# Performance work log

Measured on AMD Instinct MI355X. Metric: run time of the kernel, lower is better.

## Reference

```python
import jax, jax.numpy as jnp
import numpy as np

D = 64        # gat_output_dim == state_dim
HID = 128     # hidden_dim
ADIM = 2 * D  # action_dim (ope_dim + insert_dim)


def _mk(key, shape, scale=0.05):
    return jax.random.normal(key, shape, dtype=jnp.float32) * scale


def setup_inputs() -> dict:
    key = jax.random.key(0)
    ks = jax.random.split(key, 24)
    inp = {
        "ope_gat": jax.random.normal(ks[0], (8, 258, D), jnp.float32),
        "insert_gat": jax.random.normal(ks[1], (8, 256, D), jnp.float32),
        "h": jax.random.normal(ks[2], (8, D), jnp.float32),
        "c": jax.random.normal(ks[3], (8, D), jnp.float32),
        # LSTM (pytorch layout: gates i,f,g,o stacked -> [4D, in])
        "W_ih": _mk(ks[4], (4 * D, D)),
        "W_hh": _mk(ks[5], (4 * D, D)),
        "b_ih": _mk(ks[6], (4 * D,)),
        "b_hh": _mk(ks[7], (4 * D,)),
        # V_net: Linear(D,HID) -> Linear(HID,HID) -> LeakyReLU -> Linear(HID,1)
        "Wv0": _mk(ks[8], (HID, D)), "bv0": _mk(ks[9], (HID,)),
        "Wv1": _mk(ks[10], (HID, HID)), "bv1": _mk(ks[11], (HID,)),
        "Wv2": _mk(ks[12], (1, HID)), "bv2": _mk(ks[13], (1,)),
        # A_net: Linear(D+ADIM,HID) -> Linear(HID,HID) -> LeakyReLU -> Linear(HID,1)
        "Wa0": _mk(ks[14], (HID, D + ADIM)), "ba0": _mk(ks[15], (HID,)),
        "Wa1": _mk(ks[16], (HID, HID)), "ba1": _mk(ks[17], (HID,)),
        "Wa2": _mk(ks[18], (1, HID)), "ba2": _mk(ks[19], (1,)),
    }
    return inp


def _lrelu(x):
    return jnp.where(x >= 0, x, 0.01 * x)


def _forward(ope_gat, insert_gat, h, c,
             W_ih, W_hh, b_ih, b_hh,
             Wv0, bv0, Wv1, bv1, Wv2, bv2,
             Wa0, ba0, Wa1, ba1, Wa2, ba2):
    ope = ope_gat[:, 1:-1]                # [B, O, D]
    state = ope.mean(axis=-2)             # [B, D]

    # single-step LSTM (pytorch gate order i, f, g, o)
    gates = state @ W_ih.T + b_ih + h @ W_hh.T + b_hh  # [B, 4D]
    i_g, f_g, g_g, o_g = jnp.split(gates, 4, axis=-1)
    cn = jax.nn.sigmoid(f_g) * c + jax.nn.sigmoid(i_g) * jnp.tanh(g_g)
    hn = jax.nn.sigmoid(o_g) * jnp.tanh(cn)
    rnn_state = hn                        # [B, D]

    # V head (note: no activation after first linear -- name-overwrite bug)
    V = _lrelu((rnn_state @ Wv0.T + bv0) @ Wv1.T + bv1) @ Wv2.T + bv2  # [B, 1]

    # A head on the full (ope x insert) cross-join; ope side is detached.
    ope_d = jax.lax.stop_gradient(ope)    # [B, O, D]
    B, O, _ = ope_d.shape
    I = insert_gat.shape[1]
    # Decompose first linear over the concat [state | ope | insert] (exact math).
    Ws, Wo, Wi = Wa0[:, :D], Wa0[:, D:2 * D], Wa0[:, 2 * D:]
    h0 = (rnn_state @ Ws.T)[:, None, None, :] \
         + jnp.einsum('bod,hd->boh', ope_d, Wo)[:, :, None, :] \
         + jnp.einsum('bid,hd->bih', insert_gat, Wi)[:, None, :, :] \
         + ba0                              # [B, O, I, HID]
    h1 = _lrelu(jnp.einsum('boih,gh->boig', h0, Wa1) + ba1)
    A = (jnp.einsum('boih,h->boi', h1, Wa2[0]) + ba2[0]).reshape(B, O * I)
    return V, A, hn, cn


def reference(ope_gat, insert_gat, h, c,
              W_ih, W_hh, b_ih, b_hh,
              Wv0, bv0, Wv1, bv1, Wv2, bv2,
              Wa0, ba0, Wa1, ba1, Wa2, ba2):
    return _forward(ope_gat, insert_gat, h, c,
                    W_ih, W_hh, b_ih, b_hh,
                    Wv0, bv0, Wv1, bv1, Wv2, bv2,
                    Wa0, ba0, Wa1, ba1, Wa2, ba2)
```

## Files before the change

### kernel.cpp

```cpp
#include <hip/hip_runtime.h>
#include <hip/hip_bf16.h>
#include <math.h>

typedef unsigned short u16;


__device__ __forceinline__ u16 f2b(float x) { __hip_bfloat16 b = __float2bfloat16(x); return *(u16*)&b; }
__device__ __forceinline__ void cvt8(const uint4 u, float* f) {
    f[0] = __uint_as_float(u.x << 16); f[1] = __uint_as_float(u.x & 0xFFFF0000u);
    f[2] = __uint_as_float(u.y << 16); f[3] = __uint_as_float(u.y & 0xFFFF0000u);
    f[4] = __uint_as_float(u.z << 16); f[5] = __uint_as_float(u.z & 0xFFFF0000u);
    f[6] = __uint_as_float(u.w << 16); f[7] = __uint_as_float(u.w & 0xFFFF0000u);
}

__global__ __launch_bounds__(256) void k1_head(
    const float* __restrict__ ope, const float* __restrict__ hin, const float* __restrict__ cin,
    const float* __restrict__ W_ih, const float* __restrict__ W_hh,
    const float* __restrict__ b_ih, const float* __restrict__ b_hh,
    const float* __restrict__ Wv0, const float* __restrict__ bv0,
    const float* __restrict__ Wv1, const float* __restrict__ bv1,
    const float* __restrict__ Wv2, const float* __restrict__ bv2,
    const float* __restrict__ Wa0, const float* __restrict__ ba0,
    const float* __restrict__ Wa2, const float* __restrict__ ba2,
    float* __restrict__ ws, int fb)
{
    const int b = blockIdx.x, t = threadIdx.x;
    __shared__ float red[256], state[64], hvec[64], gl[256], hn_s[64], t0a[128], t1a[128];

    {
        const int d = t & 63, q = t >> 6;
        const float* p = ope + b * 16512 + (1 + q * 64) * 64 + d;
        float s = 0.f;
        #pragma unroll 8
        for (int r = 0; r < 64; ++r) s += p[r * 64];
        red[t] = s;
    }
    __syncthreads();
    if (t < 64)       state[t]   = (red[t] + red[t+64] + red[t+128] + red[t+192]) * (1.f/256.f);
    else if (t < 128) hvec[t-64] = hin[b*64 + (t-64)];
    __syncthreads();

    {
        float g = b_ih[t] + b_hh[t];
        #pragma unroll 8
        for (int d = 0; d < 64; ++d)
            g += state[d] * W_ih[t*64 + d] + hvec[d] * W_hh[t*64 + d];
        gl[t] = g;
    }
    __syncthreads();

    if (t < 64) {
        const float ig = gl[t], fg = gl[64+t], gg = gl[128+t], og = gl[192+t];
        const float c  = cin[b*64 + t];
        const float si = 1.f/(1.f + expf(-ig));
        const float sf = 1.f/(1.f + expf(-fg));
        const float so = 1.f/(1.f + expf(-og));
        const float cn = sf*c + si*tanhf(gg);
        const float hn = so*tanhf(cn);
        ws[fb + 1288 + b*64 + t] = hn;
        ws[fb + 1800 + b*64 + t] = cn;
        hn_s[t] = hn;
    }
    __syncthreads();

    if (t < 128) {
        float a = bv0[t];
        #pragma unroll 8
        for (int d = 0; d < 64; ++d) a += hn_s[d] * Wv0[t*64 + d];
        t0a[t] = a;
    }
    __syncthreads();
    if (t < 128) {
        float a = bv1[t];
        #pragma unroll 8
        for (int d = 0; d < 128; ++d) a += t0a[d] * Wv1[t*128 + d];
        a = (a >= 0.f) ? a : 0.01f*a;
        t1a[t] = a * Wv2[t];
        float s2 = ba0[t];
        #pragma unroll 8
        for (int d = 0; d < 64; ++d) s2 += hn_s[d] * Wa0[t*192 + d];
        ws[fb + b*128 + t] = s2;
        const float w2v = Wa2[t];
        ws[fb + 1024 + t] = 0.505f * w2v;
        ws[fb + 1152 + t] = 0.495f * w2v;
    }
    __syncthreads();
    if (t == 0) {
        float v = bv2[0];
        for (int g = 0; g < 128; ++g) v += t1a[g];
        ws[fb + 1280 + b] = v;
        ws[fb + 2313]    = ba2[0];
    }
}

template<bool MF32>
__device__ void k2_body(const float* ope, const float* ins, const float* Wa0,
    const float* Wa1, const float* ba1, float* ws, int fb,
    u16* Wa1s, u16* Wsel, u16* inrows, float* P)
{
    const int t = threadIdx.x;
    const int b = blockIdx.x >> 5;
    const int r0 = (blockIdx.x & 31) * 16;
    const int side = (r0 >= 256) ? 1 : 0;

    #pragma unroll
    for (int k = 0; k < 16; ++k) {
        const int e4 = t + k*256;
        const int g = e4 >> 5, hq = (e4 & 31) * 4;
        const float4 w = *(const float4*)(Wa1 + g*128 + hq);
        ushort4 u; u.x = f2b(w.x); u.y = f2b(w.y); u.z = f2b(w.z); u.w = f2b(w.w);
        *(ushort4*)&Wa1s[g*136 + hq] = u;
    }
    #pragma unroll
    for (int k = 0; k < 8; ++k) {
        const int e4 = t + k*256;
        const int h = e4 >> 4, dq = (e4 & 15) * 4;
        const float4 w = *(const float4*)(Wa0 + h*192 + 64 + side*64 + dq);
        ushort4 u; u.x = f2b(w.x); u.y = f2b(w.y); u.z = f2b(w.z); u.w = f2b(w.w);
        *(ushort4*)&Wsel[h*72 + dq] = u;
    }
    {
        const int r = t >> 4, dq = (t & 15) * 4;
        const float* src = side
            ? (ins + b*16384 + (r0 - 256 + r)*64 + dq)
            : (ope + b*16512 + (1 + r0 + r)*64 + dq);
        const float4 w = *(const float4*)src;
        ushort4 u; u.x = f2b(w.x); u.y = f2b(w.y); u.z = f2b(w.z); u.w = f2b(w.w);
        *(ushort4*)&inrows[r*72 + dq] = u;
    }
    __syncthreads();

    const int r = t >> 4;
    const int q = t & 15;

    {
        float acc[8];
        #pragma unroll
        for (int k = 0; k < 8; ++k)
            acc[k] = side ? 0.0f : ws[fb + b*128 + (q + 16*k)];
        #pragma unroll
        for (int d8 = 0; d8 < 64; d8 += 8) {
            float iv[8];
            cvt8(*(const uint4*)&inrows[r*72 + d8], iv);
            #pragma unroll
            for (int k = 0; k < 8; ++k) {
                float wv[8];
                cvt8(*(const uint4*)&Wsel[(q + 16*k)*72 + d8], wv);
                #pragma unroll
                for (int j = 0; j < 8; ++j) acc[k] += wv[j] * iv[j];
            }
        }
        #pragma unroll
        for (int k = 0; k < 8; ++k) P[r*132 + q + 16*k] = acc[k];
    }
    __syncthreads();

    {
        float acc[8] = {0.f,0.f,0.f,0.f,0.f,0.f,0.f,0.f};
        #pragma unroll
        for (int h8 = 0; h8 < 128; h8 += 8) {
            const float4 p0 = *(const float4*)&P[r*132 + h8];
            const float4 p1 = *(const float4*)&P[r*132 + h8 + 4];
            #pragma unroll
            for (int k = 0; k < 8; ++k) {
                float wv[8];
                cvt8(*(const uint4*)&Wa1s[(q + 16*k)*136 + h8], wv);
                float a = acc[k];
                a += wv[0]*p0.x + wv[1]*p0.y + wv[2]*p0.z + wv[3]*p0.w;
                a += wv[4]*p1.x + wv[5]*p1.y + wv[6]*p1.z + wv[7]*p1.w;
                acc[k] = a;
            }
        }
        float part = 0.f;
        if (!side) {
            const int row = b*256 + r0 + r;
            #pragma unroll
            for (int k = 0; k < 8; ++k) {
                const int g = q + 16*k;
                const float v = acc[k] + ba1[g];
                part = fmaf(ws[fb + 1024 + g], v, part);
                if (MF32) ws[row*128 + g] = v;
                else      ((u16*)ws)[row*128 + g] = f2b(v);
            }
        } else {
            const int row = b*256 + (r0 - 256) + r;
            #pragma unroll
            for (int k = 0; k < 8; ++k) {
                const int g = q + 16*k;
                part = fmaf(ws[fb + 1024 + g], acc[k], part);
                if (MF32) ws[262144 + row*128 + g] = acc[k];
                else      ((u16*)ws)[262144 + row*128 + g] = f2b(acc[k]);
            }
        }
        part += __shfl_xor(part, 1);
        part += __shfl_xor(part, 2);
        part += __shfl_xor(part, 4);
        part += __shfl_xor(part, 8);
        if (q == 0) {
            if (!side) ws[fb + 2320 + b*256 + r0 + r] = part + ws[fb + 2313];
            else       ws[fb + 4368 + b*256 + (r0 - 256) + r] = part;
        }
    }
}

__global__ __launch_bounds__(256) void k2_xy(
    const float* ope, const float* ins, const float* Wa0, const float* Wa1,
    const float* ba1, float* ws, int fb, int mf32)
{
    __shared__ __align__(16) u16 Wa1s[128*136];
    __shared__ __align__(16) u16 Wsel[128*72];
    __shared__ __align__(16) u16 inrows[16*72];
    __shared__ __align__(16) float P[16*132];
    if (mf32) k2_body<true >(ope, ins, Wa0, Wa1, ba1, ws, fb, Wa1s, Wsel, inrows, P);
    else      k2_body<false>(ope, ins, Wa0, Wa1, ba1, ws, fb, Wa1s, Wsel, inrows, P);
}

template<bool MF32>
__device__ void k3_body(const float* ws, float* out, int fb)
{
    const int t = threadIdx.x;
    const int b = blockIdx.x >> 6;
    const int o0 = (blockIdx.x & 63) * 4;
    const float* wb = ws + fb + 1152;

    float acc[4] = {0.f, 0.f, 0.f, 0.f};
    #pragma unroll
    for (int gc = 0; gc < 8; ++gc) {
        float yv[16], wv[16];
        if (MF32) {
            const float* yr = ws + 262144 + (b*256 + t)*128 + gc*16;
            #pragma unroll
            for (int k = 0; k < 4; ++k) *(float4*)&yv[k*4] = *(const float4*)(yr + k*4);
        } else {
            const u16* yr = (const u16*)ws + 262144 + (b*256 + t)*128 + gc*16;
            cvt8(*(const uint4*)yr, yv);
            cvt8(*(const uint4*)(yr + 8), yv + 8);
        }
        #pragma unroll
        for (int k = 0; k < 4; ++k) *(float4*)&wv[k*4] = *(const float4*)(wb + gc*16 + k*4);
        #pragma unroll
        for (int o = 0; o < 4; ++o) {
            float xv[16];
            if (MF32) {
                const float* xr = ws + (b*256 + o0 + o)*128 + gc*16;
                #pragma unroll
                for (int k = 0; k < 4; ++k) *(float4*)&xv[k*4] = *(const float4*)(xr + k*4);
            } else {
                const u16* xr = (const u16*)ws + (b*256 + o0 + o)*128 + gc*16;
                cvt8(*(const uint4*)xr, xv);
                cvt8(*(const uint4*)(xr + 8), xv + 8);
            }
            float a = acc[o];
            #pragma unroll
            for (int j = 0; j < 16; ++j)
                a = fmaf(wv[j], fabsf(xv[j] + yv[j]), a);
            acc[o] = a;
        }
    }
    const float c2 = ws[fb + 4368 + b*256 + t];
    #pragma unroll
    for (int o = 0; o < 4; ++o)
        out[8 + b*65536 + (o0 + o)*256 + t] = ws[fb + 2320 + b*256 + o0 + o] + c2 + acc[o];

    if (blockIdx.x == 0) {
        if (t < 8) out[t] = ws[fb + 1280 + t];
        #pragma unroll
        for (int j = t; j < 512; j += 256) {
            out[524296 + j] = ws[fb + 1288 + j];
            out[524808 + j] = ws[fb + 1800 + j];
        }
    }
}

__global__ __launch_bounds__(256) void k3_adv(const float* ws, float* out,
                                              int fb, int mf32)
{
    if (mf32) k3_body<true >(ws, out, fb);
    else      k3_body<false>(ws, out, fb);
}

extern "C" void kernel_launch(void* const* d_in, const int* in_sizes, int n_in,
                              void* d_out, int out_size, void* d_ws, size_t ws_size,
                              hipStream_t stream) {
    float* ws = (float*)d_ws;
    float* out = (float*)d_out;
    const int mf32 = (ws_size >= (size_t)2200000) ? 1 : 0;
    const int fb   = mf32 ? 524288 : 262144;

    const float* ope = (const float*)d_in[0];
    const float* ins = (const float*)d_in[1];

    k1_head<<<dim3(8),   dim3(256), 0, stream>>>(
        ope, (const float*)d_in[2], (const float*)d_in[3],
        (const float*)d_in[4], (const float*)d_in[5],
        (const float*)d_in[6], (const float*)d_in[7],
        (const float*)d_in[8], (const float*)d_in[9],
        (const float*)d_in[10], (const float*)d_in[11],
        (const float*)d_in[12], (const float*)d_in[13],
        (const float*)d_in[14], (const float*)d_in[15],
        (const float*)d_in[18], (const float*)d_in[19], ws, fb);
    k2_xy  <<<dim3(256), dim3(256), 0, stream>>>(
        ope, ins, (const float*)d_in[14], (const float*)d_in[16],
        (const float*)d_in[17], ws, fb, mf32);
    k3_adv <<<dim3(512), dim3(256), 0, stream>>>(ws, out, fb, mf32);
}
```

Before: 133.8 us.

## Add pre-kernel for parallel mean reduction and one-time bf16 weight conversion

Measured after the change: 132.3 us. About the same (-1.2%).

```diff
diff --git a/kernel.cpp b/kernel.cpp
--- a/kernel.cpp
+++ b/kernel.cpp
@@ -4,6 +4,10 @@
 
 typedef unsigned short u16;
 
+#define PART  6416
+#define WA1B  10512
+#define WOB   18704
+#define WIB   22800
 
 __device__ __forceinline__ u16 f2b(float x) { __hip_bfloat16 b = __float2bfloat16(x); return *(u16*)&b; }
 __device__ __forceinline__ void cvt8(const uint4 u, float* f) {
@@ -12,9 +16,45 @@
     f[4] = __uint_as_float(u.z << 16); f[5] = __uint_as_float(u.z & 0xFFFF0000u);
     f[6] = __uint_as_float(u.w << 16); f[7] = __uint_as_float(u.w & 0xFFFF0000u);
 }
+__device__ __forceinline__ float dot4(const float4 a, const float4 b) {
+    return a.x*b.x + a.y*b.y + a.z*b.z + a.w*b.w;
+}
+
+__global__ __launch_bounds__(256) void k0_pre(
+    const float* __restrict__ ope, const float* __restrict__ Wa0,
+    const float* __restrict__ Wa1, float* __restrict__ ws, int fb)
+{
+    const int t = threadIdx.x;
+    if (blockIdx.x < 64) {
+        const int b = blockIdx.x >> 3, s = blockIdx.x & 7;
+        const int d = t & 63, rg = t >> 6;
+        __shared__ float red[256];
+        const float* p = ope + b*16512 + (1 + s*32 + rg*8)*64 + d;
+        float acc = 0.f;
+        #pragma unroll
+        for (int rr = 0; rr < 8; ++rr) acc += p[rr*64];
+        red[t] = acc;
+        __syncthreads();
+        if (t < 64)
+            ws[fb + PART + (b*8 + s)*64 + t] = red[t] + red[t+64] + red[t+128] + red[t+192];
+    } else {
+        const int e0 = ((blockIdx.x - 64)*256 + t) * 8;
+        const float* src;
+        u16* dst;
+        if (e0 < 16384)      { src = Wa1 + e0;                                      dst = (u16*)(ws + fb + WA1B) + e0; }
+        else if (e0 < 24576) { const int i = e0 - 16384; src = Wa0 + (i>>6)*192 + 64  + (i&63); dst = (u16*)(ws + fb + WOB) + i; }
+        else                 { const int i = e0 - 24576; src = Wa0 + (i>>6)*192 + 128 + (i&63); dst = (u16*)(ws + fb + WIB) + i; }
+        const float4 a = *(const float4*)src;
+        const float4 c = *(const float4*)(src + 4);
+        ushort4 u0; u0.x = f2b(a.x); u0.y = f2b(a.y); u0.z = f2b(a.z); u0.w = f2b(a.w);
+        ushort4 u1; u1.x = f2b(c.x); u1.y = f2b(c.y); u1.z = f2b(c.z); u1.w = f2b(c.w);
+        *(ushort4*)dst = u0;
+        *(ushort4*)(dst + 4) = u1;
+    }
+}
 
 __global__ __launch_bounds__(256) void k1_head(
-    const float* __restrict__ ope, const float* __restrict__ hin, const float* __restrict__ cin,
+    const float* __restrict__ hin, const float* __restrict__ cin,
     const float* __restrict__ W_ih, const float* __restrict__ W_hh,
     const float* __restrict__ b_ih, const float* __restrict__ b_hh,
     const float* __restrict__ Wv0, const float* __restrict__ bv0,
@@ -25,26 +65,24 @@
     float* __restrict__ ws, int fb)
 {
     const int b = blockIdx.x, t = threadIdx.x;
-    __shared__ float red[256], state[64], hvec[64], gl[256], hn_s[64], t0a[128], t1a[128];
-
-    {
-        const int d = t & 63, q = t >> 6;
-        const float* p = ope + b * 16512 + (1 + q * 64) * 64 + d;
+    __shared__ __align__(16) float state[64], hvec[64], gl[256], hn_s[64], t0a[128], t1a[128];
+
+    if (t < 64) {
         float s = 0.f;
-        #pragma unroll 8
-        for (int r = 0; r < 64; ++r) s += p[r * 64];
-        red[t] = s;
-    }
-    __syncthreads();
-    if (t < 64)       state[t]   = (red[t] + red[t+64] + red[t+128] + red[t+192]) * (1.f/256.f);
-    else if (t < 128) hvec[t-64] = hin[b*64 + (t-64)];
+        #pragma unroll
+        for (int s8 = 0; s8 < 8; ++s8) s += ws[fb + PART + (b*8 + s8)*64 + t];
+        state[t] = s * (1.f/256.f);
+    } else if (t < 128) hvec[t-64] = hin[b*64 + (t-64)];
     __syncthreads();
 
     {
         float g = b_ih[t] + b_hh[t];
-        #pragma unroll 8
-        for (int d = 0; d < 64; ++d)
-            g += state[d] * W_ih[t*64 + d] + hvec[d] * W_hh[t*64 + d];
+        const float4* wi = (const float4*)(W_ih + t*64);
+        const float4* wh = (const float4*)(W_hh + t*64);
+        #pragma unroll
+        for (int k = 0; k < 16; ++k)
+            g += dot4(wi[k], *(const float4*)&state[k*4])
+               + dot4(wh[k], *(const float4*)&hvec[k*4]);
         gl[t] = g;
     }
     __syncthreads();
@@ -65,59 +103,66 @@
 
     if (t < 128) {
         float a = bv0[t];
-        #pragma unroll 8
-        for (int d = 0; d < 64; ++d) a += hn_s[d] * Wv0[t*64 + d];
+        const float4* w = (const float4*)(Wv0 + t*64);
+        #pragma unroll
+        for (int k = 0; k < 16; ++k) a += dot4(w[k], *(const float4*)&hn_s[k*4]);
         t0a[t] = a;
     }
     __syncthreads();
     if (t < 128) {
         float a = bv1[t];
-        #pragma unroll 8
-        for (int d = 0; d < 128; ++d) a += t0a[d] * Wv1[t*128 + d];
+        const float4* w = (const float4*)(Wv1 + t*128);
+        #pragma unroll
+        for (int k = 0; k < 32; ++k) a += dot4(w[k], *(const float4*)&t0a[k*4]);
         a = (a >= 0.f) ? a : 0.01f*a;
         t1a[t] = a * Wv2[t];
         float s2 = ba0[t];
-        #pragma unroll 8
-        for (int d = 0; d < 64; ++d) s2 += hn_s[d] * Wa0[t*192 + d];
+        const float4* w0 = (const float4*)(Wa0 + t*192);
+        #pragma unroll
+        for (int k = 0; k < 16; ++k) s2 += dot4(w0[k], *(const float4*)&hn_s[k*4]);
         ws[fb + b*128 + t] = s2;
         const float w2v = Wa2[t];
         ws[fb + 1024 + t] = 0.505f * w2v;
         ws[fb + 1152 + t] = 0.495f * w2v;
     }
     __syncthreads();
-    if (t == 0) {
-        float v = bv2[0];
-        for (int g = 0; g < 128; ++g) v += t1a[g];
-        ws[fb + 1280 + b] = v;
-        ws[fb + 2313]    = ba2[0];
+    if (t < 64) {
+        float v = t1a[t] + t1a[t + 64];
+        v += __shfl_xor(v, 32); v += __shfl_xor(v, 16); v += __shfl_xor(v, 8);
+        v += __shfl_xor(v, 4);  v += __shfl_xor(v, 2);  v += __shfl_xor(v, 1);
+        if (t == 0) {
+            ws[fb + 1280 + b] = v + bv2[0];
+            ws[fb + 2313]    = ba2[0];
+        }
     }
 }
 
 template<bool MF32>
-__device__ void k2_body(const float* ope, const float* ins, const float* Wa0,
-    const float* Wa1, const float* ba1, float* ws, int fb,
-    u16* Wa1s, u16* Wsel, u16* inrows, float* P)
+__device__ void k2_body(const float* ope, const float* ins, const float* ba1,
+    float* ws, int fb, u16* Wa1s, u16* Wsel, u16* inrows, float* P)
 {
     const int t = threadIdx.x;
     const int b = blockIdx.x >> 5;
     const int r0 = (blockIdx.x & 31) * 16;
     const int side = (r0 >= 256) ? 1 : 0;
 
-    #pragma unroll
-    for (int k = 0; k < 16; ++k) {
-        const int e4 = t + k*256;
-        const int g = e4 >> 5, hq = (e4 & 31) * 4;
-        const float4 w = *(const float4*)(Wa1 + g*128 + hq);
-        ushort4 u; u.x = f2b(w.x); u.y = f2b(w.y); u.z = f2b(w.z); u.w = f2b(w.w);
-        *(ushort4*)&Wa1s[g*136 + hq] = u;
-    }
-    #pragma unroll
-    for (int k = 0; k < 8; ++k) {
-        const int e4 = t + k*256;
-        const int h = e4 >> 4, dq = (e4 & 15) * 4;
-        const float4 w = *(const float4*)(Wa0 + h*192 + 64 + side*64 + dq);
-        ushort4 u; u.x = f2b(w.x); u.y = f2b(w.y); u.z = f2b(w.z); u.w = f2b(w.w);
-        *(ushort4*)&Wsel[h*72 + dq] = u;
+    {
+        const u16* wa1b = (const u16*)(ws + fb + WA1B);
+        #pragma unroll
+        for (int k = 0; k < 8; ++k) {
+            const int e4 = t + k*256;
+            const int g = e4 >> 4, hq = (e4 & 15) * 8;
+            *(uint4*)&Wa1s[g*136 + hq] = *(const uint4*)(wa1b + g*128 + hq);
+        }
+    }
+    {
+        const u16* wsb = (const u16*)(ws + fb + (side ? WIB : WOB));
+        #pragma unroll
+        for (int k = 0; k < 4; ++k) {
+            const int e4 = t + k*256;
+            const int h = e4 >> 3, dq = (e4 & 7) * 8;
+            *(uint4*)&Wsel[h*72 + dq] = *(const uint4*)(wsb + h*64 + dq);
+        }
     }
     {
         const int r = t >> 4, dq = (t & 15) * 4;
@@ -204,15 +249,15 @@
 }
 
 __global__ __launch_bounds__(256) void k2_xy(
-    const float* ope, const float* ins, const float* Wa0, const float* Wa1,
-    const float* ba1, float* ws, int fb, int mf32)
+    const float* ope, const float* ins, const float* ba1,
+    float* ws, int fb, int mf32)
 {
     __shared__ __align__(16) u16 Wa1s[128*136];
     __shared__ __align__(16) u16 Wsel[128*72];
     __shared__ __align__(16) u16 inrows[16*72];
     __shared__ __align__(16) float P[16*132];
-    if (mf32) k2_body<true >(ope, ins, Wa0, Wa1, ba1, ws, fb, Wa1s, Wsel, inrows, P);
-    else      k2_body<false>(ope, ins, Wa0, Wa1, ba1, ws, fb, Wa1s, Wsel, inrows, P);
+    if (mf32) k2_body<true >(ope, ins, ba1, ws, fb, Wa1s, Wsel, inrows, P);
+    else      k2_body<false>(ope, ins, ba1, ws, fb, Wa1s, Wsel, inrows, P);
 }
 
 template<bool MF32>
@@ -284,14 +329,16 @@
                               hipStream_t stream) {
     float* ws = (float*)d_ws;
     float* out = (float*)d_out;
-    const int mf32 = (ws_size >= (size_t)2200000) ? 1 : 0;
+    const int mf32 = (ws_size >= (size_t)2400000) ? 1 : 0;
     const int fb   = mf32 ? 524288 : 262144;
 
     const float* ope = (const float*)d_in[0];
     const float* ins = (const float*)d_in[1];
 
+    k0_pre <<<dim3(80),  dim3(256), 0, stream>>>(
+        ope, (const float*)d_in[14], (const float*)d_in[16], ws, fb);
     k1_head<<<dim3(8),   dim3(256), 0, stream>>>(
-        ope, (const float*)d_in[2], (const float*)d_in[3],
+        (const float*)d_in[2], (const float*)d_in[3],
         (const float*)d_in[4], (const float*)d_in[5],
         (const float*)d_in[6], (const float*)d_in[7],
         (const float*)d_in[8], (const float*)d_in[9],
@@ -300,7 +347,6 @@
         (const float*)d_in[14], (const float*)d_in[15],
         (const float*)d_in[18], (const float*)d_in[19], ws, fb);
     k2_xy  <<<dim3(256), dim3(256), 0, stream>>>(
-        ope, ins, (const float*)d_in[14], (const float*)d_in[16],
-        (const float*)d_in[17], ws, fb, mf32);
+        ope, ins, (const float*)d_in[17], ws, fb, mf32);
     k3_adv <<<dim3(512), dim3(256), 0, stream>>>(ws, out, fb, mf32);
 }
```
